# Kernel tuning notes

Measured on AMD Instinct MI355X. Metric: run time of the kernel, lower is better.

## Reference

```python
import jax, jax.numpy as jnp
import numpy as np

DIM = 768
NUM_HEADS = 12
N_TOKENS = 4096


def setup_inputs() -> dict:
    key = jax.random.key(0)
    k_x, k_qkv, k_proj, k_pb = jax.random.split(key, 4)
    x = jax.random.normal(k_x, (N_TOKENS, DIM), dtype=jnp.float32)
    # nn.Linear(dim, dim*3, bias=False): weight shape (3*dim, dim)
    w_qkv = jax.random.normal(k_qkv, (3 * DIM, DIM), dtype=jnp.float32) * (DIM ** -0.5)
    # nn.Linear(dim, dim): weight (dim, dim), bias (dim,)
    w_proj = jax.random.normal(k_proj, (DIM, DIM), dtype=jnp.float32) * (DIM ** -0.5)
    b_proj = jax.random.normal(k_pb, (DIM,), dtype=jnp.float32) * 0.01
    return {"x": x, "w_qkv": w_qkv, "w_proj": w_proj, "b_proj": b_proj}


def reference(x, w_qkv, w_proj, b_proj):
    N, C = x.shape
    H = NUM_HEADS
    hd = C // H
    scale = hd ** -0.5
    qkv = (x @ w_qkv.T).reshape(N, 3, H, hd)  # (N, 3, H, hd)
    q = qkv[:, 0]  # (N, H, hd)
    k = qkv[:, 1]
    v = qkv[:, 2]
    # full NxN score matrix per head, as in the original (non-flash) code
    attn = jnp.einsum("nhd,mhd->hnm", q, k) * scale  # (H, N, N)
    attn = jax.nn.softmax(attn, axis=-1)
    out = jnp.einsum("hnm,mhd->nhd", attn, v).reshape(N, C)  # (N, C)
    return out @ w_proj.T + b_proj
```

## Files before the change

kernel.cpp:

```cpp
#include <hip/hip_runtime.h>
#include <hip/hip_bf16.h>

typedef __bf16 bf16_t;
typedef __attribute__((ext_vector_type(8))) __bf16 bf16x8;
typedef __attribute__((ext_vector_type(4))) __bf16 bf16x4;
typedef __attribute__((ext_vector_type(4))) short s16x4;
typedef __attribute__((ext_vector_type(4))) float f32x4;
typedef __attribute__((ext_vector_type(4))) _Float16 f16x4;

#define NTOK 4096
#define DIM  768
#define NH   12
#define HD   64
#define NSPLIT 4
#define KHALF (NTOK / NSPLIT)
#define XSZ  (NTOK * DIM)
#define WQSZ (3 * DIM * DIM)
#define WPSZ (DIM * DIM)
#define SCALE_L2E 0.18033688011112042f
#define SOFTMAX_C 12.0f

__device__ __forceinline__ bf16x8 load8(const bf16_t* p) {
    return *reinterpret_cast<const bf16x8*>(p);
}
__device__ __forceinline__ void store8(bf16_t* p, bf16x8 v) {
    *reinterpret_cast<bf16x8*>(p) = v;
}
__device__ __forceinline__ void gl2lds16(const bf16_t* g, bf16_t* l) {
    __builtin_amdgcn_global_load_lds(
        (const __attribute__((address_space(1))) void*)g,
        (__attribute__((address_space(3))) void*)l, 16, 0, 0);
}

__global__ __launch_bounds__(256) void cvt_kernel(
    const float* __restrict__ x, const float* __restrict__ wq,
    const float* __restrict__ wp,
    bf16_t* __restrict__ xb, bf16_t* __restrict__ wqb, bf16_t* __restrict__ wpb)
{
    size_t i = ((size_t)blockIdx.x * 256 + threadIdx.x) * 4;
    const float* src; bf16_t* dst; size_t off;
    if (i < XSZ)             { src = x;  dst = xb;  off = i; }
    else if (i < XSZ + WQSZ) { src = wq; dst = wqb; off = i - XSZ; }
    else                     { src = wp; dst = wpb; off = i - XSZ - WQSZ; }
    float4 v = *reinterpret_cast<const float4*>(src + off);
    bf16x4 o = { (bf16_t)v.x, (bf16_t)v.y, (bf16_t)v.z, (bf16_t)v.w };
    *reinterpret_cast<bf16x4*>(dst + off) = o;
}

__global__ __launch_bounds__(256) void qkv_gemm_kernel(
    const bf16_t* __restrict__ X, const bf16_t* __restrict__ W,
    bf16_t* __restrict__ Qo, bf16_t* __restrict__ Ko, bf16_t* __restrict__ Vt)
{
    __shared__ __align__(16) bf16_t As[128 * 32];
    __shared__ __align__(16) bf16_t Bs[128 * 32];
    const int tid  = threadIdx.x;
    const int wave = tid >> 6, lane = tid & 63;
    const int lr = lane & 15, lq = lane >> 4;
    const int M0 = blockIdx.x * 128;
    const int N0 = blockIdx.y * 128;
    const int wm = (wave >> 1) * 64, wn = (wave & 1) * 64;

    const int g_row = wave * 32 + (lane >> 2);
    const int g_col = (lane & 3) * 8;

    f32x4 acc[4][4] = {};

    for (int k0 = 0; k0 < DIM; k0 += 32) {
        #pragma unroll
        for (int c = 0; c < 2; ++c) {
            gl2lds16(&X[(size_t)(M0 + g_row + c * 16) * DIM + k0 + g_col],
                     &As[(wave * 32 + c * 16) * 32]);
            gl2lds16(&W[(size_t)(N0 + g_row + c * 16) * DIM + k0 + g_col],
                     &Bs[(wave * 32 + c * 16) * 32]);
        }
        __syncthreads();
        bf16x8 af[4], bfr[4];
        #pragma unroll
        for (int i = 0; i < 4; ++i) af[i]  = load8(&As[(wm + i * 16 + lr) * 32 + lq * 8]);
        #pragma unroll
        for (int i = 0; i < 4; ++i) bfr[i] = load8(&Bs[(wn + i * 16 + lr) * 32 + lq * 8]);
        #pragma unroll
        for (int r = 0; r < 4; ++r)
            #pragma unroll
            for (int c = 0; c < 4; ++c)
                acc[r][c] = __builtin_amdgcn_mfma_f32_16x16x32_bf16(af[r], bfr[c], acc[r][c], 0, 0, 0);
        __syncthreads();
    }

    const int t = N0 / DIM;
    if (t == 2) {
        #pragma unroll
        for (int r = 0; r < 4; ++r)
            #pragma unroll
            for (int c = 0; c < 4; ++c) {
                int m0 = M0 + wm + r * 16 + lq * 4;
                int rem = N0 + wn + c * 16 + lr - 2 * DIM;
                int hh = rem >> 6, d = rem & 63;
                bf16x4 v = { (bf16_t)acc[r][c][0], (bf16_t)acc[r][c][1],
                             (bf16_t)acc[r][c][2], (bf16_t)acc[r][c][3] };
                *reinterpret_cast<bf16x4*>(&Vt[((size_t)hh * HD + d) * NTOK + m0]) = v;
            }
    } else {
        #pragma unroll
        for (int r = 0; r < 4; ++r)
            #pragma unroll
            for (int c = 0; c < 4; ++c)
                #pragma unroll
                for (int reg = 0; reg < 4; ++reg) {
                    int m = M0 + wm + r * 16 + lq * 4 + reg;
                    int rem = N0 + wn + c * 16 + lr - t * DIM;
                    int hh = rem >> 6, d = rem & 63;
                    float v = acc[r][c][reg];
                    if (t == 0) Qo[(hh * NTOK + m) * HD + d] = (bf16_t)(v * SCALE_L2E);
                    else        Ko[(hh * NTOK + m) * HD + d] = (bf16_t)v;
                }
    }
}

__global__ __launch_bounds__(512) void flash_attn_kernel(
    const bf16_t* __restrict__ Qb, const bf16_t* __restrict__ Kb,
    const bf16_t* __restrict__ Vtb, _Float16* __restrict__ Opart,
    float* __restrict__ Lpart)
{
    __shared__ __align__(16) bf16_t Ks[2][64 * 64];
    __shared__ __align__(16) bf16_t Vs[2][64 * 64];
    const int tid  = threadIdx.x;
    const int wave = tid >> 6, lane = tid & 63;
    const int lr = lane & 15, lq = lane >> 4;
    const int h  = blockIdx.y;
    const int q0 = blockIdx.x * 256;
    const int sp = blockIdx.z;
    const int kt0 = sp * KHALF;
    const int NIT = KHALF / 64;

    const int kc0 = (lq ^ (lr & 7)) * 8;
    const int kc1 = ((4 + lq) ^ (lr & 7)) * 8;
    int vc[4];
    #pragma unroll
    for (int g = 0; g < 4; ++g)
        vc[g] = ((2 * g + (lq >> 1)) ^ (lr & 7)) * 8 + (lq & 1) * 4;

    const int srow = lane >> 3;
    const int scol = ((lane & 7) ^ srow) * 8;
    const bf16_t* kbase = &Kb[(size_t)h * NTOK * HD];
    const bf16_t* vbase = &Vtb[(size_t)h * HD * NTOK];
    const size_t kof = (size_t)(wave * 8 + srow) * HD + scol;
    const size_t vof = (size_t)(wave * 8 + srow) * NTOK + scol;
    const int ldw = (wave * 8) * 64;

    const bf16_t* qrowA = &Qb[((size_t)h * NTOK + q0 + wave * 32 + lr) * HD];
    const bf16_t* qrowB = qrowA + 16 * HD;
    bf16x8 qa0 = load8(&qrowA[lq * 8]);
    bf16x8 qa1 = load8(&qrowA[32 + lq * 8]);
    bf16x8 qb0 = load8(&qrowB[lq * 8]);
    bf16x8 qb1 = load8(&qrowB[32 + lq * 8]);

    f32x4 oA[4] = {}, oB[4] = {};
    f32x4 lsA = {}, lsB = {};
    const f32x4 mc = { -SOFTMAX_C, -SOFTMAX_C, -SOFTMAX_C, -SOFTMAX_C };
    const short ONE = (short)0x3F80;
    const s16x4 ones = { ONE, ONE, ONE, ONE };

    gl2lds16(kbase + (size_t)kt0 * HD + kof, &Ks[0][ldw]);
    gl2lds16(vbase + kt0 + vof,              &Vs[0][ldw]);
    gl2lds16(kbase + (size_t)(kt0 + 64) * HD + kof, &Ks[1][ldw]);
    gl2lds16(vbase + (kt0 + 64) + vof,              &Vs[1][ldw]);
    __syncthreads();

    for (int it = 0; it < NIT; ++it) {
        const int buf = it & 1;

        #pragma unroll
        for (int g = 0; g < 4; ++g) {
            bf16x8 k0 = load8(&Ks[buf][(g * 16 + lr) * 64 + kc0]);
            bf16x8 k1 = load8(&Ks[buf][(g * 16 + lr) * 64 + kc1]);
            f32x4 za = mc, zb = mc;
            __builtin_amdgcn_s_setprio(1);
            za = __builtin_amdgcn_mfma_f32_16x16x32_bf16(k0, qa0, za, 0, 0, 0);
            za = __builtin_amdgcn_mfma_f32_16x16x32_bf16(k1, qa1, za, 0, 0, 0);
            zb = __builtin_amdgcn_mfma_f32_16x16x32_bf16(k0, qb0, zb, 0, 0, 0);
            zb = __builtin_amdgcn_mfma_f32_16x16x32_bf16(k1, qb1, zb, 0, 0, 0);
            __builtin_amdgcn_s_setprio(0);
            #pragma unroll
            for (int r = 0; r < 4; ++r) {
                za[r] = __builtin_amdgcn_exp2f(za[r]);
                zb[r] = __builtin_amdgcn_exp2f(zb[r]);
            }
            bf16x4 pa = { (bf16_t)za[0], (bf16_t)za[1],
                          (bf16_t)za[2], (bf16_t)za[3] };
            bf16x4 pb = { (bf16_t)zb[0], (bf16_t)zb[1],
                          (bf16_t)zb[2], (bf16_t)zb[3] };
            s16x4 psa = __builtin_bit_cast(s16x4, pa);
            s16x4 psb = __builtin_bit_cast(s16x4, pb);
            __builtin_amdgcn_s_setprio(1);
            lsA = __builtin_amdgcn_mfma_f32_16x16x16bf16_1k(ones, psa, lsA, 0, 0, 0);
            lsB = __builtin_amdgcn_mfma_f32_16x16x16bf16_1k(ones, psb, lsB, 0, 0, 0);
            #pragma unroll
            for (int dt = 0; dt < 4; ++dt) {
                s16x4 va = *reinterpret_cast<const s16x4*>(
                    &Vs[buf][(dt * 16 + lr) * 64 + vc[g]]);
                oA[dt] = __builtin_amdgcn_mfma_f32_16x16x16bf16_1k(va, psa, oA[dt], 0, 0, 0);
                oB[dt] = __builtin_amdgcn_mfma_f32_16x16x16bf16_1k(va, psb, oB[dt], 0, 0, 0);
            }
            __builtin_amdgcn_s_setprio(0);
        }

        if (it == NIT - 1) break;

        asm volatile("s_waitcnt lgkmcnt(0)" ::: "memory");
        __builtin_amdgcn_sched_barrier(0);
        __builtin_amdgcn_s_barrier();

        if (it + 2 < NIT) {
            const int kn = kt0 + (it + 2) * 64;
            gl2lds16(kbase + (size_t)kn * HD + kof, &Ks[buf][ldw]);
            gl2lds16(vbase + kn + vof,              &Vs[buf][ldw]);
            asm volatile("s_waitcnt vmcnt(2)" ::: "memory");
        } else {
            asm volatile("s_waitcnt vmcnt(0)" ::: "memory");
        }
        __builtin_amdgcn_sched_barrier(0);
        __builtin_amdgcn_s_barrier();
    }

    const float la = lsA[0], lb = lsB[0];
    const int ma = q0 + wave * 32 + lr;
    const int mb = ma + 16;
    if (lq == 0) {
        Lpart[((size_t)sp * NH + h) * NTOK + ma] = la;
        Lpart[((size_t)sp * NH + h) * NTOK + mb] = lb;
    }
    _Float16* oa = &Opart[((size_t)sp * NTOK + ma) * DIM + h * HD];
    _Float16* ob = &Opart[((size_t)sp * NTOK + mb) * DIM + h * HD];
    #pragma unroll
    for (int dt = 0; dt < 4; ++dt) {
        f16x4 va = { (_Float16)oA[dt][0], (_Float16)oA[dt][1],
                     (_Float16)oA[dt][2], (_Float16)oA[dt][3] };
        f16x4 vb = { (_Float16)oB[dt][0], (_Float16)oB[dt][1],
                     (_Float16)oB[dt][2], (_Float16)oB[dt][3] };
        *reinterpret_cast<f16x4*>(&oa[dt * 16 + lq * 4]) = va;
        *reinterpret_cast<f16x4*>(&ob[dt * 16 + lq * 4]) = vb;
    }
}

__global__ __launch_bounds__(256) void combine_kernel(
    const _Float16* __restrict__ Opart, const float* __restrict__ Lpart,
    bf16_t* __restrict__ Ab)
{
    int idx = blockIdx.x * 256 + threadIdx.x;
    int m = idx / (DIM / 4);
    int c = (idx - m * (DIM / 4)) * 4;
    int hh = c >> 6;
    float l = 0.f;
    #pragma unroll
    for (int s = 0; s < NSPLIT; ++s)
        l += Lpart[((size_t)s * NH + hh) * NTOK + m];
    float rv = 1.f / l;
    float a0 = 0.f, a1 = 0.f, a2 = 0.f, a3 = 0.f;
    #pragma unroll
    for (int s = 0; s < NSPLIT; ++s) {
        f16x4 v = *reinterpret_cast<const f16x4*>(
            &Opart[((size_t)s * NTOK + m) * DIM + c]);
        a0 += (float)v[0]; a1 += (float)v[1];
        a2 += (float)v[2]; a3 += (float)v[3];
    }
    bf16x4 o = { (bf16_t)(a0 * rv), (bf16_t)(a1 * rv),
                 (bf16_t)(a2 * rv), (bf16_t)(a3 * rv) };
    *reinterpret_cast<bf16x4*>(&Ab[(size_t)m * DIM + c]) = o;
}

__global__ __launch_bounds__(256) void proj_gemm_kernel(
    const bf16_t* __restrict__ A, const bf16_t* __restrict__ W,
    const float* __restrict__ bias, float* __restrict__ out)
{
    __shared__ __align__(16) bf16_t As[64 * 32];
    __shared__ __align__(16) bf16_t Bs[64 * 32];
    const int tid  = threadIdx.x;
    const int wave = tid >> 6, lane = tid & 63;
    const int lr = lane & 15, lq = lane >> 4;
    const int M0 = blockIdx.x * 64;
    const int N0 = blockIdx.y * 64;
    const int wr = (wave >> 1) * 32, wc = (wave & 1) * 32;
    const int g_row = tid >> 2;
    const int g_col = (tid & 3) * 8;

    f32x4 acc[2][2] = {};

    for (int k0 = 0; k0 < DIM; k0 += 32) {
        gl2lds16(&A[(size_t)(M0 + g_row) * DIM + k0 + g_col], &As[wave * 512]);
        gl2lds16(&W[(size_t)(N0 + g_row) * DIM + k0 + g_col], &Bs[wave * 512]);
        __syncthreads();
        bf16x8 a0 = load8(&As[(wr + lr) * 32 + lq * 8]);
        bf16x8 a1 = load8(&As[(wr + 16 + lr) * 32 + lq * 8]);
        bf16x8 b0 = load8(&Bs[(wc + lr) * 32 + lq * 8]);
        bf16x8 b1 = load8(&Bs[(wc + 16 + lr) * 32 + lq * 8]);
        acc[0][0] = __builtin_amdgcn_mfma_f32_16x16x32_bf16(a0, b0, acc[0][0], 0, 0, 0);
        acc[0][1] = __builtin_amdgcn_mfma_f32_16x16x32_bf16(a0, b1, acc[0][1], 0, 0, 0);
        acc[1][0] = __builtin_amdgcn_mfma_f32_16x16x32_bf16(a1, b0, acc[1][0], 0, 0, 0);
        acc[1][1] = __builtin_amdgcn_mfma_f32_16x16x32_bf16(a1, b1, acc[1][1], 0, 0, 0);
        __syncthreads();
    }

    #pragma unroll
    for (int r = 0; r < 2; ++r)
        #pragma unroll
        for (int c = 0; c < 2; ++c)
            #pragma unroll
            for (int reg = 0; reg < 4; ++reg) {
                int m = M0 + wr + r * 16 + lq * 4 + reg;
                int n = N0 + wc + c * 16 + lr;
                out[(size_t)m * DIM + n] = acc[r][c][reg] + bias[n];
            }
}

extern "C" void kernel_launch(void* const* d_in, const int* in_sizes, int n_in,
                              void* d_out, int out_size, void* d_ws, size_t ws_size,
                              hipStream_t stream)
{
    const float* x      = (const float*)d_in[0];
    const float* w_qkv  = (const float*)d_in[1];
    const float* w_proj = (const float*)d_in[2];
    const float* b_proj = (const float*)d_in[3];
    float* out = (float*)d_out;

    char* ws = (char*)d_ws;
    const size_t sz = (size_t)NH * NTOK * HD * sizeof(bf16_t);
    bf16_t*   Q     = (bf16_t*)(ws);
    bf16_t*   K     = (bf16_t*)(ws + sz);
    bf16_t*   Vt    = (bf16_t*)(ws + 2 * sz);
    bf16_t*   xb    = (bf16_t*)(ws + 3 * sz);
    bf16_t*   wqb   = (bf16_t*)(ws + 3 * sz + (size_t)XSZ * 2);
    bf16_t*   wpb   = (bf16_t*)(ws + 3 * sz + (size_t)(XSZ + WQSZ) * 2);
    _Float16* Opart = (_Float16*)(ws + 3 * sz + (size_t)(XSZ + WQSZ + WPSZ) * 2);
    float*    Lpart = (float*)xb;
    bf16_t*   Ab    = Q;

    cvt_kernel<<<dim3((XSZ + WQSZ + WPSZ) / 1024), 256, 0, stream>>>(
        x, w_qkv, w_proj, xb, wqb, wpb);
    qkv_gemm_kernel<<<dim3(NTOK / 128, (3 * DIM) / 128), 256, 0, stream>>>(
        xb, wqb, Q, K, Vt);
    flash_attn_kernel<<<dim3(NTOK / 256, NH, NSPLIT), 512, 0, stream>>>(
        Q, K, Vt, Opart, Lpart);
    combine_kernel<<<dim3((NTOK * DIM / 4) / 256), 256, 0, stream>>>(
        Opart, Lpart, Ab);
    proj_gemm_kernel<<<dim3(NTOK / 64, DIM / 64), 256, 0, stream>>>(
        Ab, wpb, b_proj, out);
}
```

Before: 186.5 us.

## Halve flash-attention waves per block, give each wave 64 query rows

```diff
diff --git a/kernel.cpp b/kernel.cpp
--- a/kernel.cpp
+++ b/kernel.cpp
@@ -117,7 +117,7 @@
     }
 }
 
-__global__ __launch_bounds__(512) void flash_attn_kernel(
+__global__ __launch_bounds__(256) void flash_attn_kernel(
     const bf16_t* __restrict__ Qb, const bf16_t* __restrict__ Kb,
     const bf16_t* __restrict__ Vtb, _Float16* __restrict__ Opart,
     float* __restrict__ Lpart)
@@ -144,27 +144,37 @@
     const int scol = ((lane & 7) ^ srow) * 8;
     const bf16_t* kbase = &Kb[(size_t)h * NTOK * HD];
     const bf16_t* vbase = &Vtb[(size_t)h * HD * NTOK];
-    const size_t kof = (size_t)(wave * 8 + srow) * HD + scol;
-    const size_t vof = (size_t)(wave * 8 + srow) * NTOK + scol;
-    const int ldw = (wave * 8) * 64;
-
-    const bf16_t* qrowA = &Qb[((size_t)h * NTOK + q0 + wave * 32 + lr) * HD];
-    const bf16_t* qrowB = qrowA + 16 * HD;
-    bf16x8 qa0 = load8(&qrowA[lq * 8]);
-    bf16x8 qa1 = load8(&qrowA[32 + lq * 8]);
-    bf16x8 qb0 = load8(&qrowB[lq * 8]);
-    bf16x8 qb1 = load8(&qrowB[32 + lq * 8]);
-
-    f32x4 oA[4] = {}, oB[4] = {};
-    f32x4 lsA = {}, lsB = {};
+    const size_t kofA = (size_t)(wave * 16 + srow) * HD + scol;
+    const size_t kofB = kofA + (size_t)8 * HD;
+    const size_t vofA = (size_t)(wave * 16 + srow) * NTOK + scol;
+    const size_t vofB = vofA + (size_t)8 * NTOK;
+    const int ldA = (wave * 16) * 64;
+    const int ldB = (wave * 16 + 8) * 64;
+
+    const bf16_t* qrow = &Qb[((size_t)h * NTOK + q0 + wave * 64 + lr) * HD];
+    bf16x8 qa0 = load8(&qrow[lq * 8]);
+    bf16x8 qa1 = load8(&qrow[32 + lq * 8]);
+    bf16x8 qb0 = load8(&qrow[16 * HD + lq * 8]);
+    bf16x8 qb1 = load8(&qrow[16 * HD + 32 + lq * 8]);
+    bf16x8 qc0 = load8(&qrow[32 * HD + lq * 8]);
+    bf16x8 qc1 = load8(&qrow[32 * HD + 32 + lq * 8]);
+    bf16x8 qd0 = load8(&qrow[48 * HD + lq * 8]);
+    bf16x8 qd1 = load8(&qrow[48 * HD + 32 + lq * 8]);
+
+    f32x4 oA[4] = {}, oB[4] = {}, oC[4] = {}, oD[4] = {};
+    f32x4 lsA = {}, lsB = {}, lsC = {}, lsD = {};
     const f32x4 mc = { -SOFTMAX_C, -SOFTMAX_C, -SOFTMAX_C, -SOFTMAX_C };
     const short ONE = (short)0x3F80;
     const s16x4 ones = { ONE, ONE, ONE, ONE };
 
-    gl2lds16(kbase + (size_t)kt0 * HD + kof, &Ks[0][ldw]);
-    gl2lds16(vbase + kt0 + vof,              &Vs[0][ldw]);
-    gl2lds16(kbase + (size_t)(kt0 + 64) * HD + kof, &Ks[1][ldw]);
-    gl2lds16(vbase + (kt0 + 64) + vof,              &Vs[1][ldw]);
+    gl2lds16(kbase + (size_t)kt0 * HD + kofA, &Ks[0][ldA]);
+    gl2lds16(kbase + (size_t)kt0 * HD + kofB, &Ks[0][ldB]);
+    gl2lds16(vbase + kt0 + vofA,              &Vs[0][ldA]);
+    gl2lds16(vbase + kt0 + vofB,              &Vs[0][ldB]);
+    gl2lds16(kbase + (size_t)(kt0 + 64) * HD + kofA, &Ks[1][ldA]);
+    gl2lds16(kbase + (size_t)(kt0 + 64) * HD + kofB, &Ks[1][ldB]);
+    gl2lds16(vbase + (kt0 + 64) + vofA,              &Vs[1][ldA]);
+    gl2lds16(vbase + (kt0 + 64) + vofB,              &Vs[1][ldB]);
     __syncthreads();
 
     for (int it = 0; it < NIT; ++it) {
@@ -174,33 +184,45 @@
         for (int g = 0; g < 4; ++g) {
             bf16x8 k0 = load8(&Ks[buf][(g * 16 + lr) * 64 + kc0]);
             bf16x8 k1 = load8(&Ks[buf][(g * 16 + lr) * 64 + kc1]);
-            f32x4 za = mc, zb = mc;
+            f32x4 za = mc, zb = mc, zc = mc, zd = mc;
             __builtin_amdgcn_s_setprio(1);
             za = __builtin_amdgcn_mfma_f32_16x16x32_bf16(k0, qa0, za, 0, 0, 0);
             za = __builtin_amdgcn_mfma_f32_16x16x32_bf16(k1, qa1, za, 0, 0, 0);
             zb = __builtin_amdgcn_mfma_f32_16x16x32_bf16(k0, qb0, zb, 0, 0, 0);
             zb = __builtin_amdgcn_mfma_f32_16x16x32_bf16(k1, qb1, zb, 0, 0, 0);
+            zc = __builtin_amdgcn_mfma_f32_16x16x32_bf16(k0, qc0, zc, 0, 0, 0);
+            zc = __builtin_amdgcn_mfma_f32_16x16x32_bf16(k1, qc1, zc, 0, 0, 0);
+            zd = __builtin_amdgcn_mfma_f32_16x16x32_bf16(k0, qd0, zd, 0, 0, 0);
+            zd = __builtin_amdgcn_mfma_f32_16x16x32_bf16(k1, qd1, zd, 0, 0, 0);
             __builtin_amdgcn_s_setprio(0);
             #pragma unroll
             for (int r = 0; r < 4; ++r) {
                 za[r] = __builtin_amdgcn_exp2f(za[r]);
                 zb[r] = __builtin_amdgcn_exp2f(zb[r]);
+                zc[r] = __builtin_amdgcn_exp2f(zc[r]);
+                zd[r] = __builtin_amdgcn_exp2f(zd[r]);
             }
-            bf16x4 pa = { (bf16_t)za[0], (bf16_t)za[1],
-                          (bf16_t)za[2], (bf16_t)za[3] };
-            bf16x4 pb = { (bf16_t)zb[0], (bf16_t)zb[1],
-                          (bf16_t)zb[2], (bf16_t)zb[3] };
+            bf16x4 pa = { (bf16_t)za[0], (bf16_t)za[1], (bf16_t)za[2], (bf16_t)za[3] };
+            bf16x4 pb = { (bf16_t)zb[0], (bf16_t)zb[1], (bf16_t)zb[2], (bf16_t)zb[3] };
+            bf16x4 pc = { (bf16_t)zc[0], (bf16_t)zc[1], (bf16_t)zc[2], (bf16_t)zc[3] };
+            bf16x4 pd = { (bf16_t)zd[0], (bf16_t)zd[1], (bf16_t)zd[2], (bf16_t)zd[3] };
             s16x4 psa = __builtin_bit_cast(s16x4, pa);
             s16x4 psb = __builtin_bit_cast(s16x4, pb);
+            s16x4 psc = __builtin_bit_cast(s16x4, pc);
+            s16x4 psd = __builtin_bit_cast(s16x4, pd);
             __builtin_amdgcn_s_setprio(1);
             lsA = __builtin_amdgcn_mfma_f32_16x16x16bf16_1k(ones, psa, lsA, 0, 0, 0);
             lsB = __builtin_amdgcn_mfma_f32_16x16x16bf16_1k(ones, psb, lsB, 0, 0, 0);
+            lsC = __builtin_amdgcn_mfma_f32_16x16x16bf16_1k(ones, psc, lsC, 0, 0, 0);
+            lsD = __builtin_amdgcn_mfma_f32_16x16x16bf16_1k(ones, psd, lsD, 0, 0, 0);
             #pragma unroll
             for (int dt = 0; dt < 4; ++dt) {
                 s16x4 va = *reinterpret_cast<const s16x4*>(
                     &Vs[buf][(dt * 16 + lr) * 64 + vc[g]]);
                 oA[dt] = __builtin_amdgcn_mfma_f32_16x16x16bf16_1k(va, psa, oA[dt], 0, 0, 0);
                 oB[dt] = __builtin_amdgcn_mfma_f32_16x16x16bf16_1k(va, psb, oB[dt], 0, 0, 0);
+                oC[dt] = __builtin_amdgcn_mfma_f32_16x16x16bf16_1k(va, psc, oC[dt], 0, 0, 0);
+                oD[dt] = __builtin_amdgcn_mfma_f32_16x16x16bf16_1k(va, psd, oD[dt], 0, 0, 0);
             }
             __builtin_amdgcn_s_setprio(0);
         }
@@ -213,9 +235,11 @@
 
         if (it + 2 < NIT) {
             const int kn = kt0 + (it + 2) * 64;
-            gl2lds16(kbase + (size_t)kn * HD + kof, &Ks[buf][ldw]);
-            gl2lds16(vbase + kn + vof,              &Vs[buf][ldw]);
-            asm volatile("s_waitcnt vmcnt(2)" ::: "memory");
+            gl2lds16(kbase + (size_t)kn * HD + kofA, &Ks[buf][ldA]);
+            gl2lds16(kbase + (size_t)kn * HD + kofB, &Ks[buf][ldB]);
+            gl2lds16(vbase + kn + vofA,              &Vs[buf][ldA]);
+            gl2lds16(vbase + kn + vofB,              &Vs[buf][ldB]);
+            asm volatile("s_waitcnt vmcnt(4)" ::: "memory");
         } else {
             asm volatile("s_waitcnt vmcnt(0)" ::: "memory");
         }
@@ -223,23 +247,24 @@
         __builtin_amdgcn_s_barrier();
     }
 
-    const float la = lsA[0], lb = lsB[0];
-    const int ma = q0 + wave * 32 + lr;
-    const int mb = ma + 16;
+    const int mbase = q0 + wave * 64 + lr;
     if (lq == 0) {
-        Lpart[((size_t)sp * NH + h) * NTOK + ma] = la;
-        Lpart[((size_t)sp * NH + h) * NTOK + mb] = lb;
-    }
-    _Float16* oa = &Opart[((size_t)sp * NTOK + ma) * DIM + h * HD];
-    _Float16* ob = &Opart[((size_t)sp * NTOK + mb) * DIM + h * HD];
-    #pragma unroll
-    for (int dt = 0; dt < 4; ++dt) {
-        f16x4 va = { (_Float16)oA[dt][0], (_Float16)oA[dt][1],
-                     (_Float16)oA[dt][2], (_Float16)oA[dt][3] };
-        f16x4 vb = { (_Float16)oB[dt][0], (_Float16)oB[dt][1],
-                     (_Float16)oB[dt][2], (_Float16)oB[dt][3] };
-        *reinterpret_cast<f16x4*>(&oa[dt * 16 + lq * 4]) = va;
-        *reinterpret_cast<f16x4*>(&ob[dt * 16 + lq * 4]) = vb;
+        float* lp = &Lpart[((size_t)sp * NH + h) * NTOK + mbase];
+        lp[0]  = lsA[0];
+        lp[16] = lsB[0];
+        lp[32] = lsC[0];
+        lp[48] = lsD[0];
+    }
+    #pragma unroll
+    for (int s = 0; s < 4; ++s) {
+        const f32x4* o = (s == 0) ? oA : (s == 1) ? oB : (s == 2) ? oC : oD;
+        _Float16* op = &Opart[((size_t)sp * NTOK + mbase + s * 16) * DIM + h * HD];
+        #pragma unroll
+        for (int dt = 0; dt < 4; ++dt) {
+            f16x4 v = { (_Float16)o[dt][0], (_Float16)o[dt][1],
+                        (_Float16)o[dt][2], (_Float16)o[dt][3] };
+            *reinterpret_cast<f16x4*>(&op[dt * 16 + lq * 4]) = v;
+        }
     }
 }
 
@@ -339,7 +364,7 @@
         x, w_qkv, w_proj, xb, wqb, wpb);
     qkv_gemm_kernel<<<dim3(NTOK / 128, (3 * DIM) / 128), 256, 0, stream>>>(
         xb, wqb, Q, K, Vt);
-    flash_attn_kernel<<<dim3(NTOK / 256, NH, NSPLIT), 512, 0, stream>>>(
+    flash_attn_kernel<<<dim3(NTOK / 256, NH, NSPLIT), 256, 0, stream>>>(
         Q, K, Vt, Opart, Lpart);
     combine_kernel<<<dim3((NTOK * DIM / 4) / 256), 256, 0, stream>>>(
         Opart, Lpart, Ab);
```

Result: slower. 233.3 us (+25.1%).

## Switch flash attention inner loop to 32x32 MFMA tiles with scalar row sums

Applied to the files above, without the earlier changes.

```diff
diff --git a/kernel.cpp b/kernel.cpp
--- a/kernel.cpp
+++ b/kernel.cpp
@@ -6,6 +6,7 @@
 typedef __attribute__((ext_vector_type(4))) __bf16 bf16x4;
 typedef __attribute__((ext_vector_type(4))) short s16x4;
 typedef __attribute__((ext_vector_type(4))) float f32x4;
+typedef __attribute__((ext_vector_type(16))) float f32x16;
 typedef __attribute__((ext_vector_type(4))) _Float16 f16x4;
 
 #define NTOK 4096
@@ -126,19 +127,19 @@
     __shared__ __align__(16) bf16_t Vs[2][64 * 64];
     const int tid  = threadIdx.x;
     const int wave = tid >> 6, lane = tid & 63;
-    const int lr = lane & 15, lq = lane >> 4;
+    const int r31 = lane & 31, l5 = lane >> 5, r7 = lane & 7;
     const int h  = blockIdx.y;
     const int q0 = blockIdx.x * 256;
     const int sp = blockIdx.z;
     const int kt0 = sp * KHALF;
     const int NIT = KHALF / 64;
 
-    const int kc0 = (lq ^ (lr & 7)) * 8;
-    const int kc1 = ((4 + lq) ^ (lr & 7)) * 8;
-    int vc[4];
-    #pragma unroll
-    for (int g = 0; g < 4; ++g)
-        vc[g] = ((2 * g + (lq >> 1)) ^ (lr & 7)) * 8 + (lq & 1) * 4;
+    int kcol[4];
+    #pragma unroll
+    for (int s = 0; s < 4; ++s) kcol[s] = ((s * 2 + l5) ^ r7) * 8;
+    int vcol[8];
+    #pragma unroll
+    for (int o = 0; o < 8; ++o) vcol[o] = (o ^ r7) * 8 + l5 * 4;
 
     const int srow = lane >> 3;
     const int scol = ((lane & 7) ^ srow) * 8;
@@ -148,18 +149,13 @@
     const size_t vof = (size_t)(wave * 8 + srow) * NTOK + scol;
     const int ldw = (wave * 8) * 64;
 
-    const bf16_t* qrowA = &Qb[((size_t)h * NTOK + q0 + wave * 32 + lr) * HD];
-    const bf16_t* qrowB = qrowA + 16 * HD;
-    bf16x8 qa0 = load8(&qrowA[lq * 8]);
-    bf16x8 qa1 = load8(&qrowA[32 + lq * 8]);
-    bf16x8 qb0 = load8(&qrowB[lq * 8]);
-    bf16x8 qb1 = load8(&qrowB[32 + lq * 8]);
-
-    f32x4 oA[4] = {}, oB[4] = {};
-    f32x4 lsA = {}, lsB = {};
-    const f32x4 mc = { -SOFTMAX_C, -SOFTMAX_C, -SOFTMAX_C, -SOFTMAX_C };
-    const short ONE = (short)0x3F80;
-    const s16x4 ones = { ONE, ONE, ONE, ONE };
+    const bf16_t* qrow = &Qb[((size_t)h * NTOK + q0 + wave * 32 + r31) * HD];
+    bf16x8 qf[4];
+    #pragma unroll
+    for (int s = 0; s < 4; ++s) qf[s] = load8(&qrow[s * 16 + l5 * 8]);
+
+    float la = 0.f;
+    f32x16 oLo = {}, oHi = {};
 
     gl2lds16(kbase + (size_t)kt0 * HD + kof, &Ks[0][ldw]);
     gl2lds16(vbase + kt0 + vof,              &Vs[0][ldw]);
@@ -169,38 +165,39 @@
 
     for (int it = 0; it < NIT; ++it) {
         const int buf = it & 1;
-
-        #pragma unroll
-        for (int g = 0; g < 4; ++g) {
-            bf16x8 k0 = load8(&Ks[buf][(g * 16 + lr) * 64 + kc0]);
-            bf16x8 k1 = load8(&Ks[buf][(g * 16 + lr) * 64 + kc1]);
-            f32x4 za = mc, zb = mc;
+        const bf16_t* Kt = Ks[buf];
+        const bf16_t* Vv = Vs[buf];
+
+        #pragma unroll
+        for (int kh = 0; kh < 2; ++kh) {
+            const int krow = (kh * 32 + r31) * 64;
+            f32x16 z;
+            #pragma unroll
+            for (int r = 0; r < 16; ++r) z[r] = -SOFTMAX_C;
             __builtin_amdgcn_s_setprio(1);
-            za = __builtin_amdgcn_mfma_f32_16x16x32_bf16(k0, qa0, za, 0, 0, 0);
-            za = __builtin_amdgcn_mfma_f32_16x16x32_bf16(k1, qa1, za, 0, 0, 0);
-            zb = __builtin_amdgcn_mfma_f32_16x16x32_bf16(k0, qb0, zb, 0, 0, 0);
-            zb = __builtin_amdgcn_mfma_f32_16x16x32_bf16(k1, qb1, zb, 0, 0, 0);
+            #pragma unroll
+            for (int s = 0; s < 4; ++s) {
+                bf16x8 kf = load8(&Kt[krow + kcol[s]]);
+                z = __builtin_amdgcn_mfma_f32_32x32x16_bf16(kf, qf[s], z, 0, 0, 0);
+            }
             __builtin_amdgcn_s_setprio(0);
             #pragma unroll
-            for (int r = 0; r < 4; ++r) {
-                za[r] = __builtin_amdgcn_exp2f(za[r]);
-                zb[r] = __builtin_amdgcn_exp2f(zb[r]);
-            }
-            bf16x4 pa = { (bf16_t)za[0], (bf16_t)za[1],
-                          (bf16_t)za[2], (bf16_t)za[3] };
-            bf16x4 pb = { (bf16_t)zb[0], (bf16_t)zb[1],
-                          (bf16_t)zb[2], (bf16_t)zb[3] };
-            s16x4 psa = __builtin_bit_cast(s16x4, pa);
-            s16x4 psb = __builtin_bit_cast(s16x4, pb);
+            for (int r = 0; r < 16; ++r) {
+                z[r] = __builtin_amdgcn_exp2f(z[r]);
+                la += z[r];
+            }
             __builtin_amdgcn_s_setprio(1);
-            lsA = __builtin_amdgcn_mfma_f32_16x16x16bf16_1k(ones, psa, lsA, 0, 0, 0);
-            lsB = __builtin_amdgcn_mfma_f32_16x16x16bf16_1k(ones, psb, lsB, 0, 0, 0);
-            #pragma unroll
-            for (int dt = 0; dt < 4; ++dt) {
-                s16x4 va = *reinterpret_cast<const s16x4*>(
-                    &Vs[buf][(dt * 16 + lr) * 64 + vc[g]]);
-                oA[dt] = __builtin_amdgcn_mfma_f32_16x16x16bf16_1k(va, psa, oA[dt], 0, 0, 0);
-                oB[dt] = __builtin_amdgcn_mfma_f32_16x16x16bf16_1k(va, psb, oB[dt], 0, 0, 0);
+            #pragma unroll
+            for (int o = 0; o < 4; ++o) {
+                bf16x4 p = { (bf16_t)z[4 * o], (bf16_t)z[4 * o + 1],
+                             (bf16_t)z[4 * o + 2], (bf16_t)z[4 * o + 3] };
+                s16x4 ps = __builtin_bit_cast(s16x4, p);
+                s16x4 vLo = *reinterpret_cast<const s16x4*>(
+                    &Vv[r31 * 64 + vcol[kh * 4 + o]]);
+                s16x4 vHi = *reinterpret_cast<const s16x4*>(
+                    &Vv[(32 + r31) * 64 + vcol[kh * 4 + o]]);
+                oLo = __builtin_amdgcn_mfma_f32_32x32x8bf16_1k(vLo, ps, oLo, 0, 0, 0);
+                oHi = __builtin_amdgcn_mfma_f32_32x32x8bf16_1k(vHi, ps, oHi, 0, 0, 0);
             }
             __builtin_amdgcn_s_setprio(0);
         }
@@ -223,23 +220,21 @@
         __builtin_amdgcn_s_barrier();
     }
 
-    const float la = lsA[0], lb = lsB[0];
-    const int ma = q0 + wave * 32 + lr;
-    const int mb = ma + 16;
-    if (lq == 0) {
-        Lpart[((size_t)sp * NH + h) * NTOK + ma] = la;
-        Lpart[((size_t)sp * NH + h) * NTOK + mb] = lb;
-    }
-    _Float16* oa = &Opart[((size_t)sp * NTOK + ma) * DIM + h * HD];
-    _Float16* ob = &Opart[((size_t)sp * NTOK + mb) * DIM + h * HD];
-    #pragma unroll
-    for (int dt = 0; dt < 4; ++dt) {
-        f16x4 va = { (_Float16)oA[dt][0], (_Float16)oA[dt][1],
-                     (_Float16)oA[dt][2], (_Float16)oA[dt][3] };
-        f16x4 vb = { (_Float16)oB[dt][0], (_Float16)oB[dt][1],
-                     (_Float16)oB[dt][2], (_Float16)oB[dt][3] };
-        *reinterpret_cast<f16x4*>(&oa[dt * 16 + lq * 4]) = va;
-        *reinterpret_cast<f16x4*>(&ob[dt * 16 + lq * 4]) = vb;
+    la += __shfl_xor(la, 32);
+    const int m = q0 + wave * 32 + r31;
+    if (l5 == 0)
+        Lpart[((size_t)sp * NH + h) * NTOK + m] = la;
+
+    _Float16* op = &Opart[((size_t)sp * NTOK + m) * DIM + h * HD];
+    #pragma unroll
+    for (int t = 0; t < 4; ++t) {
+        const int d0 = 8 * t + 4 * l5;
+        f16x4 vlo = { (_Float16)oLo[4 * t],     (_Float16)oLo[4 * t + 1],
+                      (_Float16)oLo[4 * t + 2], (_Float16)oLo[4 * t + 3] };
+        f16x4 vhi = { (_Float16)oHi[4 * t],     (_Float16)oHi[4 * t + 1],
+                      (_Float16)oHi[4 * t + 2], (_Float16)oHi[4 * t + 3] };
+        *reinterpret_cast<f16x4*>(&op[d0])      = vlo;
+        *reinterpret_cast<f16x4*>(&op[32 + d0]) = vhi;
     }
 }
 
```

New measurement: 190.0 us. Within noise of the previous version (+1.8%).
